# Optimization experiments

Hardware: AMD Instinct MI355X
Metric: run time of the kernel (lower is better)

## Reference

```python
import jax, jax.numpy as jnp
import numpy as np

B, H, W, C = 16, 128, 128, 64
PH, PW = 2, 2  # pool_size == strides, 'valid' padding


def setup_inputs() -> dict:
    key = jax.random.key(0)
    k0, k1, k2, k3 = jax.random.split(key, 4)
    shp = (B, H, W, C)
    return {
        "x0": jax.random.normal(k0, shp, dtype=jnp.float32),
        "x1": jax.random.normal(k1, shp, dtype=jnp.float32),
        "x2": jax.random.normal(k2, shp, dtype=jnp.float32),
        "x3": jax.random.normal(k3, shp, dtype=jnp.float32),
    }


def _windows(t, ph, pw):
    # (B,H,W,C,...) -> (B, H//ph, W//pw, C, ph*pw, ...) with row-major window
    # flattening (h then w), matching tf.nn.max_pool_with_argmax index order.
    b, h, w, c = t.shape[:4]
    rest = t.shape[4:]
    t = t.reshape((b, h // ph, ph, w // pw, pw, c) + rest)
    perm = (0, 1, 3, 5, 2, 4) + tuple(range(6, 6 + len(rest)))
    t = t.transpose(perm)
    return t.reshape((b, h // ph, w // pw, c, ph * pw) + rest)


def reference(x0, x1, x2, x3):
    # Stack quaternion components: (B,H,W,C,4)
    x = jnp.stack([x0, x1, x2, x3], axis=-1)
    # Euclidean norm over the 4 components: (B,H,W,C)
    norm = jnp.sqrt(jnp.sum(x * x, axis=-1))
    # Non-overlapping 2x2 windows (pool_size == strides, VALID padding)
    norm_w = _windows(norm, PH, PW)           # (B,Ho,Wo,C,4win)
    idx = jnp.argmax(norm_w, axis=-1)         # first-max tie-break, like TF
    x_w = _windows(x, PH, PW)                 # (B,Ho,Wo,C,4win,4comp)
    pooled = jnp.take_along_axis(x_w, idx[..., None, None], axis=4)
    pooled = pooled.squeeze(4)                # (B,Ho,Wo,C,4comp)
    return (pooled[..., 0], pooled[..., 1], pooled[..., 2], pooled[..., 3])


if __name__ == "__main__":
    out = reference(**setup_inputs())
    print([o.shape for o in out])
```

## Files before the change

kernel.cpp:

```cpp
#include <hip/hip_runtime.h>

#define BN 16
#define HN 128
#define WN 128
#define CN 64
#define HO 64
#define WO 64
#define C4 16
#define ROW4 (WN * C4)
#define OUTQ (BN * HO * WO * C4)

typedef float f32x4 __attribute__((ext_vector_type(4)));

__device__ __forceinline__ f32x4 qnorm4(const f32x4 a, const f32x4 b,
                                        const f32x4 c, const f32x4 d) {
#pragma clang fp contract(off)
    f32x4 r;
    r.x = sqrtf(((a.x * a.x + b.x * b.x) + c.x * c.x) + d.x * d.x);
    r.y = sqrtf(((a.y * a.y + b.y * b.y) + c.y * c.y) + d.y * d.y);
    r.z = sqrtf(((a.z * a.z + b.z * b.z) + c.z * c.z) + d.z * d.z);
    r.w = sqrtf(((a.w * a.w + b.w * b.w) + c.w * c.w) + d.w * d.w);
    return r;
}

__device__ __forceinline__ f32x4 ntload(const f32x4* __restrict__ p) {
    return __builtin_nontemporal_load(p);
}

__device__ __forceinline__ f32x4 shfl16(f32x4 v) {
    f32x4 r;
    r.x = __shfl_xor(v.x, 16);
    r.y = __shfl_xor(v.y, 16);
    r.z = __shfl_xor(v.z, 16);
    r.w = __shfl_xor(v.w, 16);
    return r;
}

#define VERT(f, k)                                                             \
    do {                                                                       \
        bool m = n1.f > n0.f;                                                  \
        bn.f = m ? n1.f : n0.f;                                                \
        s0.f = m ? a0r1.f : a0r0.f;                                            \
        s1.f = m ? a1r1.f : a1r0.f;                                            \
        s2.f = m ? a2r1.f : a2r0.f;                                            \
        s3.f = m ? a3r1.f : a3r0.f;                                            \
        rows |= (m ? (1 << (k)) : 0);                                          \
    } while (0)

#define HORZ(f, k)                                                             \
    do {                                                                       \
        bool rE = (rows >> (k)) & 1;                                           \
        bool rO = (rowsO >> (k)) & 1;                                          \
        bool tO = (bnO.f > bn.f) || ((bnO.f == bn.f) && rE && !rO);            \
        s0.f = tO ? p0.f : s0.f;                                               \
        s1.f = tO ? p1.f : s1.f;                                               \
        s2.f = tO ? p2.f : s2.f;                                               \
        s3.f = tO ? p3.f : s3.f;                                               \
    } while (0)

__global__ __launch_bounds__(256) void maxnorm_pool_kernel(
    const f32x4* __restrict__ x0, const f32x4* __restrict__ x1,
    const f32x4* __restrict__ x2, const f32x4* __restrict__ x3,
    f32x4* __restrict__ out) {
    const int t = blockIdx.x * 256 + threadIdx.x;
    const int within = t & (ROW4 - 1);
    const int rowIdx = t >> 11;
    const int ho = rowIdx & (HO - 1);
    const int b  = rowIdx >> 6;

    const int g0 = (b * HN + 2 * ho) * ROW4 + within;
    const int g1 = g0 + ROW4;

    f32x4 a0r0 = ntload(x0 + g0), a1r0 = ntload(x1 + g0);
    f32x4 a2r0 = ntload(x2 + g0), a3r0 = ntload(x3 + g0);
    f32x4 a0r1 = ntload(x0 + g1), a1r1 = ntload(x1 + g1);
    f32x4 a2r1 = ntload(x2 + g1), a3r1 = ntload(x3 + g1);

    f32x4 n0 = qnorm4(a0r0, a1r0, a2r0, a3r0);
    f32x4 n1 = qnorm4(a0r1, a1r1, a2r1, a3r1);

    f32x4 bn, s0, s1, s2, s3;
    int rows = 0;
    VERT(x, 0); VERT(y, 1); VERT(z, 2); VERT(w, 3);

    f32x4 bnO = shfl16(bn);
    f32x4 p0 = shfl16(s0), p1 = shfl16(s1), p2 = shfl16(s2), p3 = shfl16(s3);
    int rowsO = __shfl_xor(rows, 16);

    HORZ(x, 0); HORZ(y, 1); HORZ(z, 2); HORZ(w, 3);

    if (((threadIdx.x >> 4) & 1) == 0) {
        const int c4 = within & (C4 - 1);
        const int wo = within >> 5;
        const int oi = ((b * HO + ho) * WO + wo) * C4 + c4;
        __builtin_nontemporal_store(s0, out + oi);
        __builtin_nontemporal_store(s1, out + OUTQ + oi);
        __builtin_nontemporal_store(s2, out + 2 * OUTQ + oi);
        __builtin_nontemporal_store(s3, out + 3 * OUTQ + oi);
    }
}

extern "C" void kernel_launch(void* const* d_in, const int* in_sizes, int n_in,
                              void* d_out, int out_size, void* d_ws, size_t ws_size,
                              hipStream_t stream) {
    const f32x4* x0 = (const f32x4*)d_in[0];
    const f32x4* x1 = (const f32x4*)d_in[1];
    const f32x4* x2 = (const f32x4*)d_in[2];
    const f32x4* x3 = (const f32x4*)d_in[3];
    f32x4* out = (f32x4*)d_out;

    const int total_threads = BN * HO * ROW4;
    const int block = 256;
    const int grid = total_threads / block;
    maxnorm_pool_kernel<<<grid, block, 0, stream>>>(x0, x1, x2, x3, out);
}
```

Measured before the change: 239.5 us.

## Have each thread reduce a full 2x2 window instead of shuffling halves

Each thread now loads all four window positions for 4 channels and does the argmax in registers with first-max tie-break order. This removes the cross-lane shuffles, the tie-break bitmask logic and the half-idle store lanes, and halves the thread count. Per-thread loads double to 16 vector loads, which raises register pressure and changes the memory access pattern: each wavefront now covers 2 contiguous segments per input row instead of one.

```diff
diff --git a/kernel.cpp b/kernel.cpp
--- a/kernel.cpp
+++ b/kernel.cpp
@@ -27,35 +27,22 @@
     return __builtin_nontemporal_load(p);
 }
 
-__device__ __forceinline__ f32x4 shfl16(f32x4 v) {
-    f32x4 r;
-    r.x = __shfl_xor(v.x, 16);
-    r.y = __shfl_xor(v.y, 16);
-    r.z = __shfl_xor(v.z, 16);
-    r.w = __shfl_xor(v.w, 16);
-    return r;
-}
-
-#define VERT(f, k)                                                             \
+#define STEP1(f, nn, b0, b1, b2, b3)                                           \
     do {                                                                       \
-        bool m = n1.f > n0.f;                                                  \
-        bn.f = m ? n1.f : n0.f;                                                \
-        s0.f = m ? a0r1.f : a0r0.f;                                            \
-        s1.f = m ? a1r1.f : a1r0.f;                                            \
-        s2.f = m ? a2r1.f : a2r0.f;                                            \
-        s3.f = m ? a3r1.f : a3r0.f;                                            \
-        rows |= (m ? (1 << (k)) : 0);                                          \
+        bool m = (nn).f > bn.f;                                                \
+        bn.f = m ? (nn).f : bn.f;                                              \
+        s0.f = m ? (b0).f : s0.f;                                              \
+        s1.f = m ? (b1).f : s1.f;                                              \
+        s2.f = m ? (b2).f : s2.f;                                              \
+        s3.f = m ? (b3).f : s3.f;                                              \
     } while (0)
 
-#define HORZ(f, k)                                                             \
+#define STEP(nn, b0, b1, b2, b3)                                               \
     do {                                                                       \
-        bool rE = (rows >> (k)) & 1;                                           \
-        bool rO = (rowsO >> (k)) & 1;                                          \
-        bool tO = (bnO.f > bn.f) || ((bnO.f == bn.f) && rE && !rO);            \
-        s0.f = tO ? p0.f : s0.f;                                               \
-        s1.f = tO ? p1.f : s1.f;                                               \
-        s2.f = tO ? p2.f : s2.f;                                               \
-        s3.f = tO ? p3.f : s3.f;                                               \
+        STEP1(x, nn, b0, b1, b2, b3);                                          \
+        STEP1(y, nn, b0, b1, b2, b3);                                          \
+        STEP1(z, nn, b0, b1, b2, b3);                                          \
+        STEP1(w, nn, b0, b1, b2, b3);                                          \
     } while (0)
 
 __global__ __launch_bounds__(256) void maxnorm_pool_kernel(
@@ -63,41 +50,40 @@
     const f32x4* __restrict__ x2, const f32x4* __restrict__ x3,
     f32x4* __restrict__ out) {
     const int t = blockIdx.x * 256 + threadIdx.x;
-    const int within = t & (ROW4 - 1);
-    const int rowIdx = t >> 11;
-    const int ho = rowIdx & (HO - 1);
-    const int b  = rowIdx >> 6;
+    const int c4 = t & (C4 - 1);
+    const int wo = (t >> 4) & (WO - 1);
+    const int row = t >> 10;
+    const int ho = row & (HO - 1);
+    const int b  = row >> 6;
 
-    const int g0 = (b * HN + 2 * ho) * ROW4 + within;
-    const int g1 = g0 + ROW4;
+    const int g00 = (b * HN + 2 * ho) * ROW4 + wo * (2 * C4) + c4;
+    const int g01 = g00 + C4;
+    const int g10 = g00 + ROW4;
+    const int g11 = g10 + C4;
 
-    f32x4 a0r0 = ntload(x0 + g0), a1r0 = ntload(x1 + g0);
-    f32x4 a2r0 = ntload(x2 + g0), a3r0 = ntload(x3 + g0);
-    f32x4 a0r1 = ntload(x0 + g1), a1r1 = ntload(x1 + g1);
-    f32x4 a2r1 = ntload(x2 + g1), a3r1 = ntload(x3 + g1);
+    f32x4 a0p0 = ntload(x0 + g00), a1p0 = ntload(x1 + g00);
+    f32x4 a2p0 = ntload(x2 + g00), a3p0 = ntload(x3 + g00);
+    f32x4 a0p1 = ntload(x0 + g01), a1p1 = ntload(x1 + g01);
+    f32x4 a2p1 = ntload(x2 + g01), a3p1 = ntload(x3 + g01);
+    f32x4 a0p2 = ntload(x0 + g10), a1p2 = ntload(x1 + g10);
+    f32x4 a2p2 = ntload(x2 + g10), a3p2 = ntload(x3 + g10);
+    f32x4 a0p3 = ntload(x0 + g11), a1p3 = ntload(x1 + g11);
+    f32x4 a2p3 = ntload(x2 + g11), a3p3 = ntload(x3 + g11);
 
-    f32x4 n0 = qnorm4(a0r0, a1r0, a2r0, a3r0);
-    f32x4 n1 = qnorm4(a0r1, a1r1, a2r1, a3r1);
+    f32x4 n0 = qnorm4(a0p0, a1p0, a2p0, a3p0);
+    f32x4 n1 = qnorm4(a0p1, a1p1, a2p1, a3p1);
+    f32x4 n2 = qnorm4(a0p2, a1p2, a2p2, a3p2);
+    f32x4 n3 = qnorm4(a0p3, a1p3, a2p3, a3p3);
 
-    f32x4 bn, s0, s1, s2, s3;
-    int rows = 0;
-    VERT(x, 0); VERT(y, 1); VERT(z, 2); VERT(w, 3);
+    f32x4 bn = n0, s0 = a0p0, s1 = a1p0, s2 = a2p0, s3 = a3p0;
+    STEP(n1, a0p1, a1p1, a2p1, a3p1);
+    STEP(n2, a0p2, a1p2, a2p2, a3p2);
+    STEP(n3, a0p3, a1p3, a2p3, a3p3);
 
-    f32x4 bnO = shfl16(bn);
-    f32x4 p0 = shfl16(s0), p1 = shfl16(s1), p2 = shfl16(s2), p3 = shfl16(s3);
-    int rowsO = __shfl_xor(rows, 16);
-
-    HORZ(x, 0); HORZ(y, 1); HORZ(z, 2); HORZ(w, 3);
-
-    if (((threadIdx.x >> 4) & 1) == 0) {
-        const int c4 = within & (C4 - 1);
-        const int wo = within >> 5;
-        const int oi = ((b * HO + ho) * WO + wo) * C4 + c4;
-        __builtin_nontemporal_store(s0, out + oi);
-        __builtin_nontemporal_store(s1, out + OUTQ + oi);
-        __builtin_nontemporal_store(s2, out + 2 * OUTQ + oi);
-        __builtin_nontemporal_store(s3, out + 3 * OUTQ + oi);
-    }
+    __builtin_nontemporal_store(s0, out + t);
+    __builtin_nontemporal_store(s1, out + OUTQ + t);
+    __builtin_nontemporal_store(s2, out + 2 * OUTQ + t);
+    __builtin_nontemporal_store(s3, out + 3 * OUTQ + t);
 }
 
 extern "C" void kernel_launch(void* const* d_in, const int* in_sizes, int n_in,
@@ -109,7 +95,7 @@
     const f32x4* x3 = (const f32x4*)d_in[3];
     f32x4* out = (f32x4*)d_out;
 
-    const int total_threads = BN * HO * ROW4;
+    const int total_threads = OUTQ;
     const int block = 256;
     const int grid = total_threads / block;
     maxnorm_pool_kernel<<<grid, block, 0, stream>>>(x0, x1, x2, x3, out);
```

After: 241.1 us. About the same (+0.6%).
